# Performance work log

Measured on AMD Instinct MI355X. Metric: run time of the kernel, lower is better.

Reference implementation:

```python
import jax, jax.numpy as jnp
import numpy as np

B, S, H, NH = 1, 2048, 2048, 32
HD = H // NH  # 64
DFF = 4 * H
EPS = 1e-5


def layer_norm(x, w, b):
    mu = jnp.mean(x, axis=-1, keepdims=True)
    var = jnp.var(x, axis=-1, keepdims=True)
    return (x - mu) * jax.lax.rsqrt(var + EPS) * w + b


def setup_inputs() -> dict:
    key = jax.random.key(0)
    ks = jax.random.split(key, 16)
    std = 0.02
    hidden_states = jax.random.normal(ks[0], (B, S, H), dtype=jnp.float32)
    # additive causal mask [1,1,S,S]
    causal = jnp.tril(jnp.ones((S, S), dtype=jnp.bool_))
    attention_mask = jnp.where(causal, 0.0, -1e9).astype(jnp.float32)[None, None]
    p = lambda k, shp: (jax.random.normal(k, shp, dtype=jnp.float32) * std)
    return {
        "hidden_states": hidden_states,
        "attention_mask": attention_mask,
        "ln1_w": jnp.ones((H,), jnp.float32), "ln1_b": jnp.zeros((H,), jnp.float32),
        "wq": p(ks[1], (H, H)), "bq": jnp.zeros((H,), jnp.float32),
        "wk": p(ks[2], (H, H)), "bk": jnp.zeros((H,), jnp.float32),
        "wv": p(ks[3], (H, H)), "bv": jnp.zeros((H,), jnp.float32),
        "wo": p(ks[4], (H, H)), "bo": jnp.zeros((H,), jnp.float32),
        "w1": p(ks[5], (H, DFF)), "b1": jnp.zeros((DFF,), jnp.float32),
        "w2": p(ks[6], (DFF, H)), "b2": jnp.zeros((H,), jnp.float32),
        "ln2_w": jnp.ones((H,), jnp.float32), "ln2_b": jnp.zeros((H,), jnp.float32),
    }


def reference(hidden_states, attention_mask, ln1_w, ln1_b, wq, bq, wk, bk, wv, bv,
              wo, bo, w1, b1, w2, b2, ln2_w, ln2_b):
    x = hidden_states
    # --- pre-norm attention ---
    residual = x
    h = layer_norm(x, ln1_w, ln1_b)
    scaling = HD ** -0.5
    q = (h @ wq + bq).reshape(B, S, NH, HD) * scaling
    k = (h @ wk + bk).reshape(B, S, NH, HD)
    v = (h @ wv + bv).reshape(B, S, NH, HD)
    scores = jnp.einsum('bqhd,bkhd->bhqk', q, k) + attention_mask
    p = jax.nn.softmax(scores, axis=-1)  # dropout is identity in eval
    attn = jnp.einsum('bhqk,bkhd->bqhd', p, v).reshape(B, S, H)
    attn = attn @ wo + bo
    x = residual + attn
    # --- pre-norm MLP ---
    residual = x
    h = layer_norm(x, ln2_w, ln2_b)
    h = jax.nn.gelu(h @ w1 + b1, approximate=False) @ w2 + b2
    return residual + h
```

## Files before the change

### kernel.cpp

```cpp
#include <hip/hip_runtime.h>
#include <math.h>

#define H 2048
#define S 2048
#define NH 32
#define HD 64
#define DFF 8192

typedef __attribute__((ext_vector_type(4))) float f32x4;
typedef __attribute__((ext_vector_type(8))) short short8;
typedef __attribute__((ext_vector_type(4))) short s16x4;

static __device__ __forceinline__ ushort f2bf(float f) {
  unsigned u = __float_as_uint(f);
  u += 0x7fff + ((u >> 16) & 1);
  return (ushort)(u >> 16);
}

static __device__ __forceinline__ void gl_lds16(const ushort* g, ushort* l) {
  __builtin_amdgcn_global_load_lds(
      (__attribute__((address_space(1))) const void*)g,
      (__attribute__((address_space(3))) void*)l, 16, 0, 0);
}

__global__ __launch_bounds__(256) void transpose_all_kernel(
    const float* __restrict__ wq, const float* __restrict__ wk,
    const float* __restrict__ wv, const float* __restrict__ wo,
    const float* __restrict__ w1, const float* __restrict__ w2,
    ushort* __restrict__ oQKV, ushort* __restrict__ oO,
    ushort* __restrict__ o1, ushort* __restrict__ o2) {
  __shared__ __align__(16) ushort tile[64][72];
  int id = blockIdx.x;
  const float* W;
  ushort* Wt;
  int K, N, bx, by;
  if (id < 4096) {
    int which = id >> 10, r = id & 1023;
    bx = r & 31; by = r >> 5; K = H; N = H;
    W = (which == 0) ? wq : (which == 1) ? wk : (which == 2) ? wv : wo;
    Wt = (which == 3) ? oO : oQKV + (size_t)which * H * H;
  } else if (id < 8192) {
    int r = id - 4096;
    bx = r & 127; by = r >> 7; K = H; N = DFF;
    W = w1; Wt = o1;
  } else {
    int r = id - 8192;
    bx = r & 31; by = r >> 5; K = DFF; N = H;
    W = w2; Wt = o2;
  }
  int n0 = bx * 64, k0 = by * 64;
  int t = threadIdx.x;
  int lk = t >> 4;
  int ln4 = (t & 15) * 4;
#pragma unroll
  for (int p = 0; p < 4; p++) {
    int k = p * 16 + lk;
    float4 v = *reinterpret_cast<const float4*>(&W[(size_t)(k0 + k) * N + n0 + ln4]);
    float vv[4] = {v.x, v.y, v.z, v.w};
#pragma unroll
    for (int i = 0; i < 4; i++) {
      int row = ln4 + i;
      int slot = ((k >> 3) ^ (row & 7));
      tile[row][(slot << 3) + (k & 7)] = f2bf(vv[i]);
    }
  }
  __syncthreads();
  int n = t >> 2;
  int kq = (t & 3) * 8;
#pragma unroll
  for (int p = 0; p < 2; p++) {
    int kk = kq + p * 32;
    int slot = ((kk >> 3) ^ (n & 7));
    short8 o = *reinterpret_cast<const short8*>(&tile[n][slot << 3]);
    *reinterpret_cast<short8*>(&Wt[(size_t)(n0 + n) * K + k0 + kk]) = o;
  }
}

__global__ __launch_bounds__(256) void ln_kernel(
    const float* __restrict__ x, const float* __restrict__ w,
    const float* __restrict__ b, ushort* __restrict__ out) {
  int row = blockIdx.x, t = threadIdx.x;
  const float4* xr = reinterpret_cast<const float4*>(x + (size_t)row * H);
  float4 v0 = xr[t * 2], v1 = xr[t * 2 + 1];
  float s = v0.x + v0.y + v0.z + v0.w + v1.x + v1.y + v1.z + v1.w;
  float q = v0.x * v0.x + v0.y * v0.y + v0.z * v0.z + v0.w * v0.w +
            v1.x * v1.x + v1.y * v1.y + v1.z * v1.z + v1.w * v1.w;
#pragma unroll
  for (int off = 32; off > 0; off >>= 1) {
    s += __shfl_down(s, off, 64);
    q += __shfl_down(q, off, 64);
  }
  __shared__ float sm[8];
  int lane = t & 63, wv = t >> 6;
  if (lane == 0) { sm[wv] = s; sm[wv + 4] = q; }
  __syncthreads();
  s = sm[0] + sm[1] + sm[2] + sm[3];
  q = sm[4] + sm[5] + sm[6] + sm[7];
  float mu = s * (1.0f / H);
  float var = q * (1.0f / H) - mu * mu;
  float rs = rsqrtf(var + 1e-5f);
  const float4* wr = reinterpret_cast<const float4*>(w);
  const float4* br = reinterpret_cast<const float4*>(b);
  float4 w0 = wr[t * 2], w1v = wr[t * 2 + 1], b0 = br[t * 2], b1v = br[t * 2 + 1];
  short8 pk;
  pk[0] = (short)f2bf((v0.x - mu) * rs * w0.x + b0.x);
  pk[1] = (short)f2bf((v0.y - mu) * rs * w0.y + b0.y);
  pk[2] = (short)f2bf((v0.z - mu) * rs * w0.z + b0.z);
  pk[3] = (short)f2bf((v0.w - mu) * rs * w0.w + b0.w);
  pk[4] = (short)f2bf((v1.x - mu) * rs * w1v.x + b1v.x);
  pk[5] = (short)f2bf((v1.y - mu) * rs * w1v.y + b1v.y);
  pk[6] = (short)f2bf((v1.z - mu) * rs * w1v.z + b1v.z);
  pk[7] = (short)f2bf((v1.w - mu) * rs * w1v.w + b1v.w);
  *reinterpret_cast<short8*>(out + (size_t)row * H + t * 8) = pk;
}

__global__ __launch_bounds__(256) void combine2_kernel(
    const float* __restrict__ res, const float* __restrict__ p0,
    const float* __restrict__ p1, const float* __restrict__ bias,
    float* __restrict__ out) {
  size_t i = (size_t)blockIdx.x * 256 + threadIdx.x;
  float4 a = reinterpret_cast<const float4*>(res)[i];
  float4 c0 = reinterpret_cast<const float4*>(p0)[i];
  float4 c1 = reinterpret_cast<const float4*>(p1)[i];
  int col = (int)((i * 4) & (H - 1));
  float4 bb = *reinterpret_cast<const float4*>(bias + col);
  float4 o;
  o.x = a.x + c0.x + c1.x + bb.x;
  o.y = a.y + c0.y + c1.y + bb.y;
  o.z = a.z + c0.z + c1.z + bb.z;
  o.w = a.w + c0.w + c1.w + bb.w;
  reinterpret_cast<float4*>(out)[i] = o;
}

__global__ __launch_bounds__(256) void combine_ln_kernel(
    const float* __restrict__ res, const float* __restrict__ p0,
    const float* __restrict__ p1, const float* __restrict__ bias,
    const float* __restrict__ lw, const float* __restrict__ lb,
    float* __restrict__ xout, ushort* __restrict__ lnout) {
  int row = blockIdx.x, t = threadIdx.x;
  const float4* rr = reinterpret_cast<const float4*>(res + (size_t)row * H);
  const float4* r0 = reinterpret_cast<const float4*>(p0 + (size_t)row * H);
  const float4* r1 = reinterpret_cast<const float4*>(p1 + (size_t)row * H);
  const float4* bb = reinterpret_cast<const float4*>(bias);
  float4 a0 = rr[t * 2], a1 = rr[t * 2 + 1];
  float4 c0 = r0[t * 2], c1 = r0[t * 2 + 1];
  float4 d0 = r1[t * 2], d1 = r1[t * 2 + 1];
  float4 e0 = bb[t * 2], e1 = bb[t * 2 + 1];
  float4 v0, v1;
  v0.x = a0.x + c0.x + d0.x + e0.x;
  v0.y = a0.y + c0.y + d0.y + e0.y;
  v0.z = a0.z + c0.z + d0.z + e0.z;
  v0.w = a0.w + c0.w + d0.w + e0.w;
  v1.x = a1.x + c1.x + d1.x + e1.x;
  v1.y = a1.y + c1.y + d1.y + e1.y;
  v1.z = a1.z + c1.z + d1.z + e1.z;
  v1.w = a1.w + c1.w + d1.w + e1.w;
  float4* xo = reinterpret_cast<float4*>(xout + (size_t)row * H);
  xo[t * 2] = v0;
  xo[t * 2 + 1] = v1;
  float s = v0.x + v0.y + v0.z + v0.w + v1.x + v1.y + v1.z + v1.w;
  float q = v0.x * v0.x + v0.y * v0.y + v0.z * v0.z + v0.w * v0.w +
            v1.x * v1.x + v1.y * v1.y + v1.z * v1.z + v1.w * v1.w;
#pragma unroll
  for (int off = 32; off > 0; off >>= 1) {
    s += __shfl_down(s, off, 64);
    q += __shfl_down(q, off, 64);
  }
  __shared__ float sm[8];
  int lane = t & 63, wv = t >> 6;
  if (lane == 0) { sm[wv] = s; sm[wv + 4] = q; }
  __syncthreads();
  s = sm[0] + sm[1] + sm[2] + sm[3];
  q = sm[4] + sm[5] + sm[6] + sm[7];
  float mu = s * (1.0f / H);
  float var = q * (1.0f / H) - mu * mu;
  float rs = rsqrtf(var + 1e-5f);
  const float4* wr = reinterpret_cast<const float4*>(lw);
  const float4* br = reinterpret_cast<const float4*>(lb);
  float4 w0 = wr[t * 2], w1v = wr[t * 2 + 1], b0 = br[t * 2], b1v = br[t * 2 + 1];
  short8 pk;
  pk[0] = (short)f2bf((v0.x - mu) * rs * w0.x + b0.x);
  pk[1] = (short)f2bf((v0.y - mu) * rs * w0.y + b0.y);
  pk[2] = (short)f2bf((v0.z - mu) * rs * w0.z + b0.z);
  pk[3] = (short)f2bf((v0.w - mu) * rs * w0.w + b0.w);
  pk[4] = (short)f2bf((v1.x - mu) * rs * w1v.x + b1v.x);
  pk[5] = (short)f2bf((v1.y - mu) * rs * w1v.y + b1v.y);
  pk[6] = (short)f2bf((v1.z - mu) * rs * w1v.z + b1v.z);
  pk[7] = (short)f2bf((v1.w - mu) * rs * w1v.w + b1v.w);
  *reinterpret_cast<short8*>(lnout + (size_t)row * H + t * 8) = pk;
}

template <int MODE, int NI>
__global__ __launch_bounds__(512, 2) void gemm256_kernel(
    const ushort* __restrict__ A, const ushort* __restrict__ Bt,
    const float* __restrict__ bias, const float* __restrict__ biasB,
    const float* __restrict__ biasC,
    ushort* __restrict__ outb, ushort* __restrict__ outbV,
    float* __restrict__ outf,
    int M, int N, int lda, int kbeg, int klen) {
  constexpr int BN = NI * 64;
  constexpr int NH0 = (NI + 1) / 2;
  constexpr int NH1 = NI - NH0;
  constexpr int BQ0 = (NI + 1) / 2;
  __shared__ __align__(16) ushort As[2][256 * 64];
  __shared__ __align__(16) ushort Bs[2][BN * 64];
  int tid = threadIdx.x, lane = tid & 63, w = tid >> 6;
  int lm = lane & 15, kg = lane >> 4;
  int wr = w >> 2, wc = w & 3;
  int gx = gridDim.x, nwg = gx * gridDim.y;
  int orig = blockIdx.y * gx + blockIdx.x;
  int wg = (orig & 7) * (nwg >> 3) + (orig >> 3);
  int m0 = (wg % gx) * 256, n0 = (wg / gx) * BN;
  int kb0 = kbeg + blockIdx.z * klen;

  f32x4 acc[8][NI] = {};

  const ushort* srcA[4];
  const ushort* srcB[NI];
  int dbase[4];
#pragma unroll
  for (int q = 0; q < 4; q++) {
    int g = q * 512 + tid;
    int row = g >> 3, gc = g & 7;
    int col = (gc ^ (row & 7)) << 3;
    srcA[q] = A + (size_t)(m0 + row) * lda + kb0 + col;
    if (q < NI) srcB[q] = Bt + (size_t)(n0 + row) * lda + kb0 + col;
    dbase[q] = (q * 512 + w * 64) * 8;
  }

  const ushort* aB0 = &As[0][(wr * 128 + lm) * 64 + ((kg ^ (lm & 7)) << 3)];
  const ushort* aB1 = &As[0][(wr * 128 + lm) * 64 + (((4 + kg) ^ (lm & 7)) << 3)];
  const ushort* bB0 = &Bs[0][(wc * 16 * NI + lm) * 64 + ((kg ^ (lm & 7)) << 3)];
  const ushort* bB1 = &Bs[0][(wc * 16 * NI + lm) * 64 + (((4 + kg) ^ (lm & 7)) << 3)];

  int nK = klen >> 6;
#pragma unroll
  for (int q = 0; q < NI; q++) gl_lds16(srcB[q], &Bs[0][dbase[q]]);
  gl_lds16(srcA[0], &As[0][dbase[0]]);
  gl_lds16(srcA[2], &As[0][dbase[2]]);
  gl_lds16(srcA[1], &As[0][dbase[1]]);
  gl_lds16(srcA[3], &As[0][dbase[3]]);
  asm volatile("s_waitcnt vmcnt(2)" ::: "memory");
  __builtin_amdgcn_s_barrier();

  for (int kt = 0; kt < nK; kt++) {
    int cur = kt & 1, nxt = cur ^ 1;
    bool hn = (kt + 1 < nK);
    int ko = (kt + 1) << 6;
    const ushort* a0 = aB0 + cur * 16384;
    const ushort* a1 = aB1 + cur * 16384;
    const ushort* b0 = bB0 + cur * (BN * 64);
    const ushort* b1 = bB1 + cur * (BN * 64);

    short8 af[4][2], bf0[NH0][2], bf1[NH0][2];

#pragma unroll
    for (int i = 0; i < 4; i++) {
      af[i][0] = *reinterpret_cast<const short8*>(a0 + i * 1024);
      af[i][1] = *reinterpret_cast<const short8*>(a1 + i * 1024);
    }
#pragma unroll
    for (int n = 0; n < NH0; n++) {
      bf0[n][0] = *reinterpret_cast<const short8*>(b0 + n * 1024);
      bf0[n][1] = *reinterpret_cast<const short8*>(b1 + n * 1024);
    }
    if (hn) {
#pragma unroll
      for (int q = 0; q < BQ0; q++) gl_lds16(srcB[q] + ko, &Bs[nxt][dbase[q]]);
    }
    __builtin_amdgcn_s_barrier();
    __builtin_amdgcn_s_setprio(1);
#pragma unroll
    for (int i = 0; i < 4; i++)
#pragma unroll
      for (int n = 0; n < NH0; n++)
#pragma unroll
        for (int s = 0; s < 2; s++)
          acc[i][n] = __builtin_amdgcn_mfma_f32_16x16x32_bf16(af[i][s], bf0[n][s], acc[i][n], 0, 0, 0);
    __builtin_amdgcn_s_setprio(0);
    __builtin_amdgcn_s_barrier();

#pragma unroll
    for (int n = 0; n < NH1; n++) {
      bf1[n][0] = *reinterpret_cast<const short8*>(b0 + (NH0 + n) * 1024);
      bf1[n][1] = *reinterpret_cast<const short8*>(b1 + (NH0 + n) * 1024);
    }
    if (hn) {
#pragma unroll
      for (int q = BQ0; q < NI; q++) gl_lds16(srcB[q] + ko, &Bs[nxt][dbase[q]]);
    }
    __builtin_amdgcn_s_barrier();
    __builtin_amdgcn_s_setprio(1);
#pragma unroll
    for (int i = 0; i < 4; i++)
#pragma unroll
      for (int n = 0; n < NH1; n++)
#pragma unroll
        for (int s = 0; s < 2; s++)
          acc[i][NH0 + n] = __builtin_amdgcn_mfma_f32_16x16x32_bf16(af[i][s], bf1[n][s], acc[i][NH0 + n], 0, 0, 0);
    __builtin_amdgcn_s_setprio(0);
    if (hn) {
      if constexpr (NI == 4) asm volatile("s_waitcnt vmcnt(4)" ::: "memory");
      else if constexpr (NI == 3) asm volatile("s_waitcnt vmcnt(3)" ::: "memory");
      else asm volatile("s_waitcnt vmcnt(2)" ::: "memory");
    } else {
      asm volatile("s_waitcnt vmcnt(0)" ::: "memory");
    }
    __builtin_amdgcn_s_barrier();

#pragma unroll
    for (int i = 0; i < 4; i++) {
      af[i][0] = *reinterpret_cast<const short8*>(a0 + 4096 + i * 1024);
      af[i][1] = *reinterpret_cast<const short8*>(a1 + 4096 + i * 1024);
    }
    if (hn) {
      gl_lds16(srcA[0] + ko, &As[nxt][dbase[0]]);
      gl_lds16(srcA[2] + ko, &As[nxt][dbase[2]]);
    }
    __builtin_amdgcn_s_barrier();
    __builtin_amdgcn_s_setprio(1);
#pragma unroll
    for (int i = 0; i < 4; i++)
#pragma unroll
      for (int n = 0; n < NH0; n++)
#pragma unroll
        for (int s = 0; s < 2; s++)
          acc[4 + i][n] = __builtin_amdgcn_mfma_f32_16x16x32_bf16(af[i][s], bf0[n][s], acc[4 + i][n], 0, 0, 0);
    __builtin_amdgcn_s_setprio(0);
    __builtin_amdgcn_s_barrier();

    if (hn) {
      gl_lds16(srcA[1] + ko, &As[nxt][dbase[1]]);
      gl_lds16(srcA[3] + ko, &As[nxt][dbase[3]]);
    }
    __builtin_amdgcn_s_barrier();
    __builtin_amdgcn_s_setprio(1);
#pragma unroll
    for (int i = 0; i < 4; i++)
#pragma unroll
      for (int n = 0; n < NH1; n++)
#pragma unroll
        for (int s = 0; s < 2; s++)
          acc[4 + i][NH0 + n] = __builtin_amdgcn_mfma_f32_16x16x32_bf16(af[i][s], bf1[n][s], acc[4 + i][NH0 + n], 0, 0, 0);
    __builtin_amdgcn_s_setprio(0);
    if (hn) asm volatile("s_waitcnt vmcnt(2)" ::: "memory");
    __builtin_amdgcn_s_barrier();
  }

#pragma unroll
  for (int mi = 0; mi < 8; mi++) {
#pragma unroll
    for (int ni = 0; ni < NI; ni++) {
      int row0 = m0 + wr * 128 + mi * 16 + kg * 4;
      int col = n0 + wc * 16 * NI + ni * 16 + lm;
      f32x4 v4 = acc[mi][ni];
      if (MODE == 0) {
        if (col < 2 * H) {
          float bb = (col < H) ? bias[col] : biasB[col - H];
          float sc = (col < H) ? 0.125f : 1.0f;
          size_t base = (size_t)(col >> 11) * ((size_t)S * H) + (col & (H - 1));
#pragma unroll
          for (int r = 0; r < 4; r++)
            outb[base + (size_t)(row0 + r) * H] = f2bf((v4[r] + bb) * sc);
        } else {
          float bb = biasC[col - 2 * H];
          s16x4 pk;
#pragma unroll
          for (int r = 0; r < 4; r++) pk[r] = (short)f2bf(v4[r] + bb);
          *reinterpret_cast<s16x4*>(outbV + (size_t)(col - 2 * H) * S + row0) = pk;
        }
      } else if (MODE == 1) {
#pragma unroll
        for (int r = 0; r < 4; r++) {
          float t = v4[r] + bias[col];
          outb[(size_t)(row0 + r) * N + col] = f2bf(0.5f * t * (1.0f + erff(t * 0.70710678118f)));
        }
      } else {
#pragma unroll
        for (int r = 0; r < 4; r++)
          outf[(size_t)blockIdx.z * M * N + (size_t)(row0 + r) * N + col] = v4[r];
      }
    }
  }
}

__global__ __launch_bounds__(512) void attn_kernel(
    const ushort* __restrict__ Q, const ushort* __restrict__ Kmat,
    const ushort* __restrict__ VT, ushort* __restrict__ ctx) {
  __shared__ __align__(16) ushort Ks[2][128 * 64];
  __shared__ __align__(16) ushort Vs[2][64 * 128];
  __shared__ __align__(16) ushort Ps[8 * 16 * 64];
  int h = blockIdx.x;
  int x = blockIdx.y;
  int tid = threadIdx.x, lane = tid & 63, w = tid >> 6;
  int lm = lane & 15, kg = lane >> 4;

  int qbA = x, qbB = 15 - x;
  int tA = x + 1;
  const int nt = 17;

  short8 qa[2];
#pragma unroll
  for (int ks = 0; ks < 2; ks++)
    qa[ks] = *reinterpret_cast<const short8*>(
        Q + (size_t)(qbA * 128 + w * 16 + lm) * H + h * 64 + ks * 32 + kg * 8);

  float m_run[4], l_run[4];
  f32x4 o_acc[4] = {};
#pragma unroll
  for (int r = 0; r < 4; r++) { m_run[r] = -1e30f; l_run[r] = 0.f; }

  auto stage = [&](int kb, int buf) {
#pragma unroll
    for (int p = 0; p < 2; p++) {
      int gbase = p * 512 + w * 64;
      int gran = gbase + lane;
      int krow = gran >> 3, gk = gran & 7;
      gl_lds16(Kmat + (size_t)(kb * 128 + krow) * H + h * 64 + ((gk ^ (krow & 7)) << 3),
               &Ks[buf][gbase * 8]);
    }
#pragma unroll
    for (int p = 0; p < 2; p++) {
      int gbase = p * 512 + w * 64;
      int gran = gbase + lane;
      int vrow = gran >> 4, gv = gran & 15;
      gl_lds16(VT + (size_t)(h * 64 + vrow) * S + kb * 128 + ((gv ^ (vrow & 15)) << 3),
               &Vs[buf][gbase * 8]);
    }
  };

  stage(0, 0);
  __syncthreads();

  for (int t = 0; t < nt; t++) {
    int cur = t & 1;
    if (t + 1 < nt) {
      int tn = t + 1;
      stage((tn < tA) ? tn : tn - tA, cur ^ 1);
    }
    bool diag = (t == tA - 1) || (t == nt - 1);

    f32x4 sacc[8] = {};
#pragma unroll
    for (int j = 0; j < 8; j++) {
      int krow = j * 16 + lm;
#pragma unroll
      for (int ks = 0; ks < 2; ks++) {
        short8 kf = *reinterpret_cast<const short8*>(
            &Ks[cur][krow * 64 + (((ks * 4 + kg) ^ (lm & 7)) << 3)]);
        sacc[j] = __builtin_amdgcn_mfma_f32_16x16x32_bf16(qa[ks], kf, sacc[j], 0, 0, 0);
      }
    }
    if (diag) {
#pragma unroll
      for (int j = 0; j < 8; j++)
#pragma unroll
        for (int r = 0; r < 4; r++)
          if (j * 16 + lm > w * 16 + kg * 4 + r) sacc[j][r] = -1e30f;
    }

#pragma unroll
    for (int r = 0; r < 4; r++) {
      float mx = sacc[0][r];
#pragma unroll
      for (int j = 1; j < 8; j++) mx = fmaxf(mx, sacc[j][r]);
      mx = fmaxf(mx, __shfl_xor(mx, 1, 64));
      mx = fmaxf(mx, __shfl_xor(mx, 2, 64));
      mx = fmaxf(mx, __shfl_xor(mx, 4, 64));
      mx = fmaxf(mx, __shfl_xor(mx, 8, 64));
      float mnew = fmaxf(m_run[r], mx);
      float sc = __expf(m_run[r] - mnew);
      m_run[r] = mnew;
      float ps = 0.f;
#pragma unroll
      for (int j = 0; j < 8; j++) {
        float p = __expf(sacc[j][r] - mnew);
        sacc[j][r] = p;
        ps += p;
      }
      ps += __shfl_xor(ps, 1, 64);
      ps += __shfl_xor(ps, 2, 64);
      ps += __shfl_xor(ps, 4, 64);
      ps += __shfl_xor(ps, 8, 64);
      l_run[r] = l_run[r] * sc + ps;
#pragma unroll
      for (int jd = 0; jd < 4; jd++) o_acc[jd][r] *= sc;
    }

#pragma unroll
    for (int c = 0; c < 2; c++) {
#pragma unroll
      for (int jj = 0; jj < 4; jj++)
#pragma unroll
        for (int r = 0; r < 4; r++) {
          int rl = kg * 4 + r;
          int col = jj * 16 + lm;
          Ps[w * 1024 + rl * 64 + (((col >> 3) ^ (rl & 7)) << 3) + (col & 7)] =
              f2bf(sacc[c * 4 + jj][r]);
        }
      short8 pa[2];
#pragma unroll
      for (int ks = 0; ks < 2; ks++)
        pa[ks] = *reinterpret_cast<const short8*>(
            &Ps[w * 1024 + lm * 64 + (((ks * 4 + kg) ^ (lm & 7)) << 3)]);
#pragma unroll
      for (int jd = 0; jd < 4; jd++) {
        int d = jd * 16 + lm;
#pragma unroll
        for (int ks = 0; ks < 2; ks++) {
          short8 vf = *reinterpret_cast<const short8*>(
              &Vs[cur][d * 128 + (((c * 8 + ks * 4 + kg) ^ lm) << 3)]);
          o_acc[jd] = __builtin_amdgcn_mfma_f32_16x16x32_bf16(pa[ks], vf, o_acc[jd], 0, 0, 0);
        }
      }
    }

    if (t == tA - 1) {
#pragma unroll
      for (int jd = 0; jd < 4; jd++)
#pragma unroll
        for (int r = 0; r < 4; r++)
          ctx[(size_t)(qbA * 128 + w * 16 + kg * 4 + r) * H + h * 64 + jd * 16 + lm] =
              f2bf(o_acc[jd][r] / l_run[r]);
#pragma unroll
      for (int r = 0; r < 4; r++) { m_run[r] = -1e30f; l_run[r] = 0.f; }
#pragma unroll
      for (int jd = 0; jd < 4; jd++) o_acc[jd] = f32x4{0.f, 0.f, 0.f, 0.f};
#pragma unroll
      for (int ks = 0; ks < 2; ks++)
        qa[ks] = *reinterpret_cast<const short8*>(
            Q + (size_t)(qbB * 128 + w * 16 + lm) * H + h * 64 + ks * 32 + kg * 8);
    }
    __syncthreads();
  }

#pragma unroll
  for (int jd = 0; jd < 4; jd++)
#pragma unroll
    for (int r = 0; r < 4; r++)
      ctx[(size_t)(qbB * 128 + w * 16 + kg * 4 + r) * H + h * 64 + jd * 16 + lm] =
          f2bf(o_acc[jd][r] / l_run[r]);
}

extern "C" void kernel_launch(void* const* d_in, const int* in_sizes, int n_in,
                              void* d_out, int out_size, void* d_ws, size_t ws_size,
                              hipStream_t stream) {
  const float* x = (const float*)d_in[0];
  const float* ln1w = (const float*)d_in[2];
  const float* ln1b = (const float*)d_in[3];
  const float* wq = (const float*)d_in[4];
  const float* bq = (const float*)d_in[5];
  const float* wk = (const float*)d_in[6];
  const float* bk = (const float*)d_in[7];
  const float* wv = (const float*)d_in[8];
  const float* bv = (const float*)d_in[9];
  const float* wo = (const float*)d_in[10];
  const float* bo = (const float*)d_in[11];
  const float* w1 = (const float*)d_in[12];
  const float* b1 = (const float*)d_in[13];
  const float* w2 = (const float*)d_in[14];
  const float* b2 = (const float*)d_in[15];
  const float* ln2w = (const float*)d_in[16];
  const float* ln2b = (const float*)d_in[17];
  float* out = (float*)d_out;

  char* ws = (char*)d_ws;
  const size_t MB = 1024 * 1024;
  const size_t SH = (size_t)S * H;
  ushort* WT_QKV = (ushort*)(ws);
  ushort* WT_O = (ushort*)(ws + 24 * MB);
  ushort* WT_1 = (ushort*)(ws + 32 * MB);
  ushort* WT_2 = (ushort*)(ws + 64 * MB);
  ushort* LNO = (ushort*)(ws + 96 * MB);
  ushort* QKVB = (ushort*)(ws + 104 * MB);
  ushort* VTb = (ushort*)(ws + 128 * MB);
  ushort* CTX = (ushort*)(ws + 136 * MB);
  float* X1 = (float*)(ws + 144 * MB);
  ushort* MID = (ushort*)(ws);
  float* SPA = (float*)(ws + 104 * MB);
  float* SPM = (float*)(ws + 32 * MB);

  transpose_all_kernel<<<12288, 256, 0, stream>>>(
      wq, wk, wv, wo, w1, w2, WT_QKV, WT_O, WT_1, WT_2);

  ln_kernel<<<S, 256, 0, stream>>>(x, ln1w, ln1b, LNO);

  gemm256_kernel<0, 3><<<dim3(S / 256, 3 * H / 192), 512, 0, stream>>>(
      LNO, WT_QKV, bq, bk, bv, QKVB, VTb, nullptr, S, 3 * H, H, 0, H);

  attn_kernel<<<dim3(NH, 8), 512, 0, stream>>>(QKVB, QKVB + SH, VTb, CTX);

  gemm256_kernel<3, 2><<<dim3(S / 256, H / 128, 2), 512, 0, stream>>>(
      CTX, WT_O, nullptr, nullptr, nullptr, nullptr, nullptr, SPA, S, H, H, 0, H / 2);
  combine_ln_kernel<<<S, 256, 0, stream>>>(x, SPA, SPA + SH, bo, ln2w, ln2b, X1, LNO);

  gemm256_kernel<1, 4><<<dim3(S / 256, DFF / 256), 512, 0, stream>>>(
      LNO, WT_1, b1, nullptr, nullptr, MID, nullptr, nullptr, S, DFF, H, 0, H);

  gemm256_kernel<3, 2><<<dim3(S / 256, H / 128, 2), 512, 0, stream>>>(
      MID, WT_2, nullptr, nullptr, nullptr, nullptr, nullptr, SPM, S, H, DFF, 0, DFF / 2);
  combine2_kernel<<<SH / 1024, 256, 0, stream>>>(X1, SPM, SPM + SH, b2, out);
}
```

Before: 396.4 us.

## Switch GEMM kernel from 16x16x32 to 32x32x16 MFMA with configurable warp tiling

```diff
diff --git a/kernel.cpp b/kernel.cpp
--- a/kernel.cpp
+++ b/kernel.cpp
@@ -8,6 +8,7 @@
 #define DFF 8192
 
 typedef __attribute__((ext_vector_type(4))) float f32x4;
+typedef __attribute__((ext_vector_type(16))) float f32x16;
 typedef __attribute__((ext_vector_type(8))) short short8;
 typedef __attribute__((ext_vector_type(4))) short s16x4;
 
@@ -190,7 +191,7 @@
   *reinterpret_cast<short8*>(lnout + (size_t)row * H + t * 8) = pk;
 }
 
-template <int MODE, int NI>
+template <int MODE, int NI, int NT>
 __global__ __launch_bounds__(512, 2) void gemm256_kernel(
     const ushort* __restrict__ A, const ushort* __restrict__ Bt,
     const float* __restrict__ bias, const float* __restrict__ biasB,
@@ -199,21 +200,27 @@
     float* __restrict__ outf,
     int M, int N, int lda, int kbeg, int klen) {
   constexpr int BN = NI * 64;
-  constexpr int NH0 = (NI + 1) / 2;
-  constexpr int NH1 = NI - NH0;
+  constexpr int WN = (2 * NI) / NT;
+  constexpr int WM = 8 / WN;
+  constexpr int MT = 8 / WM;
+  constexpr int NH0 = (NT + 1) / 2;
+  constexpr int NH1 = NT - NH0;
+  constexpr int MH0 = MT / 2;
   constexpr int BQ0 = (NI + 1) / 2;
+  static_assert(WN * NT * 32 == BN, "geom");
+  static_assert(WM * MT * 32 == 256, "geom");
   __shared__ __align__(16) ushort As[2][256 * 64];
   __shared__ __align__(16) ushort Bs[2][BN * 64];
   int tid = threadIdx.x, lane = tid & 63, w = tid >> 6;
-  int lm = lane & 15, kg = lane >> 4;
-  int wr = w >> 2, wc = w & 3;
+  int l32 = lane & 31, hi = lane >> 5;
+  int wc = w % WN, wr = w / WN;
   int gx = gridDim.x, nwg = gx * gridDim.y;
   int orig = blockIdx.y * gx + blockIdx.x;
   int wg = (orig & 7) * (nwg >> 3) + (orig >> 3);
   int m0 = (wg % gx) * 256, n0 = (wg / gx) * BN;
   int kb0 = kbeg + blockIdx.z * klen;
 
-  f32x4 acc[8][NI] = {};
+  f32x16 acc[MT][NT] = {};
 
   const ushort* srcA[4];
   const ushort* srcB[NI];
@@ -228,10 +235,15 @@
     dbase[q] = (q * 512 + w * 64) * 8;
   }
 
-  const ushort* aB0 = &As[0][(wr * 128 + lm) * 64 + ((kg ^ (lm & 7)) << 3)];
-  const ushort* aB1 = &As[0][(wr * 128 + lm) * 64 + (((4 + kg) ^ (lm & 7)) << 3)];
-  const ushort* bB0 = &Bs[0][(wc * 16 * NI + lm) * 64 + ((kg ^ (lm & 7)) << 3)];
-  const ushort* bB1 = &Bs[0][(wc * 16 * NI + lm) * 64 + (((4 + kg) ^ (lm & 7)) << 3)];
+  int x7 = l32 & 7;
+  const ushort* aP[4];
+  const ushort* bP[4];
+#pragma unroll
+  for (int kc = 0; kc < 4; kc++) {
+    int gran = (kc * 2 + hi) ^ x7;
+    aP[kc] = &As[0][(wr * MT * 32 + l32) * 64 + (gran << 3)];
+    bP[kc] = &Bs[0][(wc * NT * 32 + l32) * 64 + (gran << 3)];
+  }
 
   int nK = klen >> 6;
 #pragma unroll
@@ -247,23 +259,21 @@
     int cur = kt & 1, nxt = cur ^ 1;
     bool hn = (kt + 1 < nK);
     int ko = (kt + 1) << 6;
-    const ushort* a0 = aB0 + cur * 16384;
-    const ushort* a1 = aB1 + cur * 16384;
-    const ushort* b0 = bB0 + cur * (BN * 64);
-    const ushort* b1 = bB1 + cur * (BN * 64);
-
-    short8 af[4][2], bf0[NH0][2], bf1[NH0][2];
-
-#pragma unroll
-    for (int i = 0; i < 4; i++) {
-      af[i][0] = *reinterpret_cast<const short8*>(a0 + i * 1024);
-      af[i][1] = *reinterpret_cast<const short8*>(a1 + i * 1024);
-    }
-#pragma unroll
-    for (int n = 0; n < NH0; n++) {
-      bf0[n][0] = *reinterpret_cast<const short8*>(b0 + n * 1024);
-      bf0[n][1] = *reinterpret_cast<const short8*>(b1 + n * 1024);
-    }
+    int aoff = cur * 16384;
+    int boff = cur * (BN * 64);
+
+    short8 af[MH0][4], bf0[NH0][4], bf1[NH1 ? NH1 : 1][4];
+
+#pragma unroll
+    for (int mt = 0; mt < MH0; mt++)
+#pragma unroll
+      for (int kc = 0; kc < 4; kc++)
+        af[mt][kc] = *reinterpret_cast<const short8*>(aP[kc] + aoff + mt * 2048);
+#pragma unroll
+    for (int nt = 0; nt < NH0; nt++)
+#pragma unroll
+      for (int kc = 0; kc < 4; kc++)
+        bf0[nt][kc] = *reinterpret_cast<const short8*>(bP[kc] + boff + nt * 2048);
     if (hn) {
 #pragma unroll
       for (int q = 0; q < BQ0; q++) gl_lds16(srcB[q] + ko, &Bs[nxt][dbase[q]]);
@@ -271,20 +281,21 @@
     __builtin_amdgcn_s_barrier();
     __builtin_amdgcn_s_setprio(1);
 #pragma unroll
-    for (int i = 0; i < 4; i++)
-#pragma unroll
-      for (int n = 0; n < NH0; n++)
-#pragma unroll
-        for (int s = 0; s < 2; s++)
-          acc[i][n] = __builtin_amdgcn_mfma_f32_16x16x32_bf16(af[i][s], bf0[n][s], acc[i][n], 0, 0, 0);
+    for (int mt = 0; mt < MH0; mt++)
+#pragma unroll
+      for (int nt = 0; nt < NH0; nt++)
+#pragma unroll
+        for (int kc = 0; kc < 4; kc++)
+          acc[mt][nt] = __builtin_amdgcn_mfma_f32_32x32x16_bf16(
+              af[mt][kc], bf0[nt][kc], acc[mt][nt], 0, 0, 0);
     __builtin_amdgcn_s_setprio(0);
     __builtin_amdgcn_s_barrier();
 
 #pragma unroll
-    for (int n = 0; n < NH1; n++) {
-      bf1[n][0] = *reinterpret_cast<const short8*>(b0 + (NH0 + n) * 1024);
-      bf1[n][1] = *reinterpret_cast<const short8*>(b1 + (NH0 + n) * 1024);
-    }
+    for (int nt = 0; nt < NH1; nt++)
+#pragma unroll
+      for (int kc = 0; kc < 4; kc++)
+        bf1[nt][kc] = *reinterpret_cast<const short8*>(bP[kc] + boff + (NH0 + nt) * 2048);
     if (hn) {
 #pragma unroll
       for (int q = BQ0; q < NI; q++) gl_lds16(srcB[q] + ko, &Bs[nxt][dbase[q]]);
@@ -292,12 +303,13 @@
     __builtin_amdgcn_s_barrier();
     __builtin_amdgcn_s_setprio(1);
 #pragma unroll
-    for (int i = 0; i < 4; i++)
-#pragma unroll
-      for (int n = 0; n < NH1; n++)
-#pragma unroll
-        for (int s = 0; s < 2; s++)
-          acc[i][NH0 + n] = __builtin_amdgcn_mfma_f32_16x16x32_bf16(af[i][s], bf1[n][s], acc[i][NH0 + n], 0, 0, 0);
+    for (int mt = 0; mt < MH0; mt++)
+#pragma unroll
+      for (int nt = 0; nt < NH1; nt++)
+#pragma unroll
+        for (int kc = 0; kc < 4; kc++)
+          acc[mt][NH0 + nt] = __builtin_amdgcn_mfma_f32_32x32x16_bf16(
+              af[mt][kc], bf1[nt][kc], acc[mt][NH0 + nt], 0, 0, 0);
     __builtin_amdgcn_s_setprio(0);
     if (hn) {
       if constexpr (NI == 4) asm volatile("s_waitcnt vmcnt(4)" ::: "memory");
@@ -309,10 +321,10 @@
     __builtin_amdgcn_s_barrier();
 
 #pragma unroll
-    for (int i = 0; i < 4; i++) {
-      af[i][0] = *reinterpret_cast<const short8*>(a0 + 4096 + i * 1024);
-      af[i][1] = *reinterpret_cast<const short8*>(a1 + 4096 + i * 1024);
-    }
+    for (int mt = 0; mt < MH0; mt++)
+#pragma unroll
+      for (int kc = 0; kc < 4; kc++)
+        af[mt][kc] = *reinterpret_cast<const short8*>(aP[kc] + aoff + (MH0 + mt) * 2048);
     if (hn) {
       gl_lds16(srcA[0] + ko, &As[nxt][dbase[0]]);
       gl_lds16(srcA[2] + ko, &As[nxt][dbase[2]]);
@@ -320,12 +332,13 @@
     __builtin_amdgcn_s_barrier();
     __builtin_amdgcn_s_setprio(1);
 #pragma unroll
-    for (int i = 0; i < 4; i++)
-#pragma unroll
-      for (int n = 0; n < NH0; n++)
-#pragma unroll
-        for (int s = 0; s < 2; s++)
-          acc[4 + i][n] = __builtin_amdgcn_mfma_f32_16x16x32_bf16(af[i][s], bf0[n][s], acc[4 + i][n], 0, 0, 0);
+    for (int mt = 0; mt < MH0; mt++)
+#pragma unroll
+      for (int nt = 0; nt < NH0; nt++)
+#pragma unroll
+        for (int kc = 0; kc < 4; kc++)
+          acc[MH0 + mt][nt] = __builtin_amdgcn_mfma_f32_32x32x16_bf16(
+              af[mt][kc], bf0[nt][kc], acc[MH0 + mt][nt], 0, 0, 0);
     __builtin_amdgcn_s_setprio(0);
     __builtin_amdgcn_s_barrier();
 
@@ -336,49 +349,60 @@
     __builtin_amdgcn_s_barrier();
     __builtin_amdgcn_s_setprio(1);
 #pragma unroll
-    for (int i = 0; i < 4; i++)
-#pragma unroll
-      for (int n = 0; n < NH1; n++)
-#pragma unroll
-        for (int s = 0; s < 2; s++)
-          acc[4 + i][NH0 + n] = __builtin_amdgcn_mfma_f32_16x16x32_bf16(af[i][s], bf1[n][s], acc[4 + i][NH0 + n], 0, 0, 0);
+    for (int mt = 0; mt < MH0; mt++)
+#pragma unroll
+      for (int nt = 0; nt < NH1; nt++)
+#pragma unroll
+        for (int kc = 0; kc < 4; kc++)
+          acc[MH0 + mt][NH0 + nt] = __builtin_amdgcn_mfma_f32_32x32x16_bf16(
+              af[mt][kc], bf1[nt][kc], acc[MH0 + mt][NH0 + nt], 0, 0, 0);
     __builtin_amdgcn_s_setprio(0);
     if (hn) asm volatile("s_waitcnt vmcnt(2)" ::: "memory");
     __builtin_amdgcn_s_barrier();
   }
 
 #pragma unroll
-  for (int mi = 0; mi < 8; mi++) {
-#pragma unroll
-    for (int ni = 0; ni < NI; ni++) {
-      int row0 = m0 + wr * 128 + mi * 16 + kg * 4;
-      int col = n0 + wc * 16 * NI + ni * 16 + lm;
-      f32x4 v4 = acc[mi][ni];
+  for (int mt = 0; mt < MT; mt++) {
+#pragma unroll
+    for (int nt = 0; nt < NT; nt++) {
+      int row0 = m0 + wr * MT * 32 + mt * 32;
+      int col = n0 + wc * NT * 32 + nt * 32 + l32;
+      f32x16 v = acc[mt][nt];
       if (MODE == 0) {
         if (col < 2 * H) {
           float bb = (col < H) ? bias[col] : biasB[col - H];
           float sc = (col < H) ? 0.125f : 1.0f;
           size_t base = (size_t)(col >> 11) * ((size_t)S * H) + (col & (H - 1));
 #pragma unroll
-          for (int r = 0; r < 4; r++)
-            outb[base + (size_t)(row0 + r) * H] = f2bf((v4[r] + bb) * sc);
+          for (int r = 0; r < 16; r++) {
+            int row = row0 + (r & 3) + 8 * (r >> 2) + 4 * hi;
+            outb[base + (size_t)row * H] = f2bf((v[r] + bb) * sc);
+          }
         } else {
           float bb = biasC[col - 2 * H];
-          s16x4 pk;
-#pragma unroll
-          for (int r = 0; r < 4; r++) pk[r] = (short)f2bf(v4[r] + bb);
-          *reinterpret_cast<s16x4*>(outbV + (size_t)(col - 2 * H) * S + row0) = pk;
+#pragma unroll
+          for (int q = 0; q < 4; q++) {
+            int rowq = row0 + 8 * q + 4 * hi;
+            s16x4 pk;
+#pragma unroll
+            for (int j = 0; j < 4; j++) pk[j] = (short)f2bf(v[q * 4 + j] + bb);
+            *reinterpret_cast<s16x4*>(outbV + (size_t)(col - 2 * H) * S + rowq) = pk;
+          }
         }
       } else if (MODE == 1) {
-#pragma unroll
-        for (int r = 0; r < 4; r++) {
-          float t = v4[r] + bias[col];
-          outb[(size_t)(row0 + r) * N + col] = f2bf(0.5f * t * (1.0f + erff(t * 0.70710678118f)));
+        float bb = bias[col];
+#pragma unroll
+        for (int r = 0; r < 16; r++) {
+          int row = row0 + (r & 3) + 8 * (r >> 2) + 4 * hi;
+          float t = v[r] + bb;
+          outb[(size_t)row * N + col] = f2bf(0.5f * t * (1.0f + erff(t * 0.70710678118f)));
         }
       } else {
 #pragma unroll
-        for (int r = 0; r < 4; r++)
-          outf[(size_t)blockIdx.z * M * N + (size_t)(row0 + r) * N + col] = v4[r];
+        for (int r = 0; r < 16; r++) {
+          int row = row0 + (r & 3) + 8 * (r >> 2) + 4 * hi;
+          outf[(size_t)blockIdx.z * M * N + (size_t)row * N + col] = v[r];
+        }
       }
     }
   }
@@ -585,19 +609,19 @@
 
   ln_kernel<<<S, 256, 0, stream>>>(x, ln1w, ln1b, LNO);
 
-  gemm256_kernel<0, 3><<<dim3(S / 256, 3 * H / 192), 512, 0, stream>>>(
+  gemm256_kernel<0, 3, 3><<<dim3(S / 256, 3 * H / 192), 512, 0, stream>>>(
       LNO, WT_QKV, bq, bk, bv, QKVB, VTb, nullptr, S, 3 * H, H, 0, H);
 
   attn_kernel<<<dim3(NH, 8), 512, 0, stream>>>(QKVB, QKVB + SH, VTb, CTX);
 
-  gemm256_kernel<3, 2><<<dim3(S / 256, H / 128, 2), 512, 0, stream>>>(
+  gemm256_kernel<3, 2, 2><<<dim3(S / 256, H / 128, 2), 512, 0, stream>>>(
       CTX, WT_O, nullptr, nullptr, nullptr, nullptr, nullptr, SPA, S, H, H, 0, H / 2);
   combine_ln_kernel<<<S, 256, 0, stream>>>(x, SPA, SPA + SH, bo, ln2w, ln2b, X1, LNO);
 
-  gemm256_kernel<1, 4><<<dim3(S / 256, DFF / 256), 512, 0, stream>>>(
+  gemm256_kernel<1, 4, 2><<<dim3(S / 256, DFF / 256), 512, 0, stream>>>(
       LNO, WT_1, b1, nullptr, nullptr, MID, nullptr, nullptr, S, DFF, H, 0, H);
 
-  gemm256_kernel<3, 2><<<dim3(S / 256, H / 128, 2), 512, 0, stream>>>(
+  gemm256_kernel<3, 2, 2><<<dim3(S / 256, H / 128, 2), 512, 0, stream>>>(
       MID, WT_2, nullptr, nullptr, nullptr, nullptr, nullptr, SPM, S, H, DFF, 0, DFF / 2);
   combine2_kernel<<<SH / 1024, 256, 0, stream>>>(X1, SPM, SPM + SH, b2, out);
 }
```

Measured after the change: 398.3 us. Within noise of the previous version (+0.5%).

## Split paired causal attention blocks into one query block per workgroup with lazy rescale

Applied to the files above, without the earlier changes.

```diff
diff --git a/kernel.cpp b/kernel.cpp
--- a/kernel.cpp
+++ b/kernel.cpp
@@ -384,26 +384,24 @@
   }
 }
 
-__global__ __launch_bounds__(512) void attn_kernel(
+__global__ __launch_bounds__(512, 4) void attn_kernel(
     const ushort* __restrict__ Q, const ushort* __restrict__ Kmat,
     const ushort* __restrict__ VT, ushort* __restrict__ ctx) {
   __shared__ __align__(16) ushort Ks[2][128 * 64];
   __shared__ __align__(16) ushort Vs[2][64 * 128];
   __shared__ __align__(16) ushort Ps[8 * 16 * 64];
   int h = blockIdx.x;
-  int x = blockIdx.y;
+  int z = blockIdx.y;
+  int qb = (z < 8) ? z : 23 - z;
   int tid = threadIdx.x, lane = tid & 63, w = tid >> 6;
   int lm = lane & 15, kg = lane >> 4;
-
-  int qbA = x, qbB = 15 - x;
-  int tA = x + 1;
-  const int nt = 17;
+  int nt = qb + 1;
 
   short8 qa[2];
 #pragma unroll
   for (int ks = 0; ks < 2; ks++)
     qa[ks] = *reinterpret_cast<const short8*>(
-        Q + (size_t)(qbA * 128 + w * 16 + lm) * H + h * 64 + ks * 32 + kg * 8);
+        Q + (size_t)(qb * 128 + w * 16 + lm) * H + h * 64 + ks * 32 + kg * 8);
 
   float m_run[4], l_run[4];
   f32x4 o_acc[4] = {};
@@ -434,11 +432,8 @@
 
   for (int t = 0; t < nt; t++) {
     int cur = t & 1;
-    if (t + 1 < nt) {
-      int tn = t + 1;
-      stage((tn < tA) ? tn : tn - tA, cur ^ 1);
-    }
-    bool diag = (t == tA - 1) || (t == nt - 1);
+    if (t + 1 < nt) stage(t + 1, cur ^ 1);
+    bool diag = (t == nt - 1);
 
     f32x4 sacc[8] = {};
 #pragma unroll
@@ -468,13 +463,13 @@
       mx = fmaxf(mx, __shfl_xor(mx, 2, 64));
       mx = fmaxf(mx, __shfl_xor(mx, 4, 64));
       mx = fmaxf(mx, __shfl_xor(mx, 8, 64));
-      float mnew = fmaxf(m_run[r], mx);
-      float sc = __expf(m_run[r] - mnew);
-      m_run[r] = mnew;
+      float mold = m_run[r];
+      bool need = (mx - mold) > 8.0f;
+      float mref = need ? mx : mold;
       float ps = 0.f;
 #pragma unroll
       for (int j = 0; j < 8; j++) {
-        float p = __expf(sacc[j][r] - mnew);
+        float p = __expf(sacc[j][r] - mref);
         sacc[j][r] = p;
         ps += p;
       }
@@ -482,9 +477,15 @@
       ps += __shfl_xor(ps, 2, 64);
       ps += __shfl_xor(ps, 4, 64);
       ps += __shfl_xor(ps, 8, 64);
-      l_run[r] = l_run[r] * sc + ps;
-#pragma unroll
-      for (int jd = 0; jd < 4; jd++) o_acc[jd][r] *= sc;
+      if (need) {
+        float sc = __expf(mold - mx);
+        m_run[r] = mx;
+        l_run[r] = l_run[r] * sc + ps;
+#pragma unroll
+        for (int jd = 0; jd < 4; jd++) o_acc[jd][r] *= sc;
+      } else {
+        l_run[r] = l_run[r] + ps;
+      }
     }
 
 #pragma unroll
@@ -514,23 +515,6 @@
         }
       }
     }
-
-    if (t == tA - 1) {
-#pragma unroll
-      for (int jd = 0; jd < 4; jd++)
-#pragma unroll
-        for (int r = 0; r < 4; r++)
-          ctx[(size_t)(qbA * 128 + w * 16 + kg * 4 + r) * H + h * 64 + jd * 16 + lm] =
-              f2bf(o_acc[jd][r] / l_run[r]);
-#pragma unroll
-      for (int r = 0; r < 4; r++) { m_run[r] = -1e30f; l_run[r] = 0.f; }
-#pragma unroll
-      for (int jd = 0; jd < 4; jd++) o_acc[jd] = f32x4{0.f, 0.f, 0.f, 0.f};
-#pragma unroll
-      for (int ks = 0; ks < 2; ks++)
-        qa[ks] = *reinterpret_cast<const short8*>(
-            Q + (size_t)(qbB * 128 + w * 16 + lm) * H + h * 64 + ks * 32 + kg * 8);
-    }
     __syncthreads();
   }
 
@@ -538,7 +522,7 @@
   for (int jd = 0; jd < 4; jd++)
 #pragma unroll
     for (int r = 0; r < 4; r++)
-      ctx[(size_t)(qbB * 128 + w * 16 + kg * 4 + r) * H + h * 64 + jd * 16 + lm] =
+      ctx[(size_t)(qb * 128 + w * 16 + kg * 4 + r) * H + h * 64 + jd * 16 + lm] =
           f2bf(o_acc[jd][r] / l_run[r]);
 }
 
@@ -588,7 +572,7 @@
   gemm256_kernel<0, 3><<<dim3(S / 256, 3 * H / 192), 512, 0, stream>>>(
       LNO, WT_QKV, bq, bk, bv, QKVB, VTb, nullptr, S, 3 * H, H, 0, H);
 
-  attn_kernel<<<dim3(NH, 8), 512, 0, stream>>>(QKVB, QKVB + SH, VTb, CTX);
+  attn_kernel<<<dim3(NH, 16), 512, 0, stream>>>(QKVB, QKVB + SH, VTb, CTX);
 
   gemm256_kernel<3, 2><<<dim3(S / 256, H / 128, 2), 512, 0, stream>>>(
       CTX, WT_O, nullptr, nullptr, nullptr, nullptr, nullptr, SPA, S, H, H, 0, H / 2);
```

Result: no change. 402.6 us (+1.6%).
